# Kernel optimization log

Hardware: AMD Instinct MI355X
Metric: run time of the kernel (lower is better)

The kernel has to match this reference:

```python
import jax, jax.numpy as jnp
import numpy as np

N_NODES = 100000
N_EDGES = 1200000
D = 64          # node_feat_size
G_FEAT = 128    # graph_feat_size
N_GRAPHS = 256
N_TASKS = 1


def setup_inputs() -> dict:
    key = jax.random.key(0)
    ks = jax.random.split(key, 12)
    node_feats = jax.random.normal(ks[0], (N_NODES, D), dtype=jnp.float32)
    edge_feats = jax.random.normal(ks[1], (N_EDGES, 8), dtype=jnp.float32)
    src = jax.random.randint(ks[2], (N_EDGES,), 0, N_NODES, dtype=jnp.int64 if jax.config.read('jax_enable_x64') else jnp.int32)
    dst = jax.random.randint(ks[3], (N_EDGES,), 0, N_NODES, dtype=src.dtype)
    graph_ids = jnp.sort(jax.random.randint(ks[4], (N_NODES,), 0, N_GRAPHS, dtype=src.dtype))
    s = 1.0 / np.sqrt(D)
    W_gcn = jax.random.uniform(ks[5], (D, D), minval=-s, maxval=s, dtype=jnp.float32)
    b_gcn = jnp.zeros((D,), jnp.float32)
    W_res = jax.random.uniform(ks[6], (D, D), minval=-s, maxval=s, dtype=jnp.float32)
    b_res = jnp.zeros((D,), jnp.float32)
    W_in = jax.random.uniform(ks[7], (D, D), minval=-s, maxval=s, dtype=jnp.float32)
    b_in = jnp.zeros((D,), jnp.float32)
    W_out = jax.random.uniform(ks[8], (D, G_FEAT), minval=-s, maxval=s, dtype=jnp.float32)
    b_out = jnp.zeros((G_FEAT,), jnp.float32)
    sp = 1.0 / np.sqrt(G_FEAT)
    W_pred = jax.random.uniform(ks[9], (G_FEAT, N_TASKS), minval=-sp, maxval=sp, dtype=jnp.float32)
    b_pred = jnp.zeros((N_TASKS,), jnp.float32)
    return dict(node_feats=node_feats, edge_feats=edge_feats, src=src, dst=dst,
                graph_ids=graph_ids, W_gcn=W_gcn, b_gcn=b_gcn, W_res=W_res, b_res=b_res,
                W_in=W_in, b_in=b_in, W_out=W_out, b_out=b_out, W_pred=W_pred, b_pred=b_pred)


def reference(node_feats, edge_feats, src, dst, graph_ids,
              W_gcn, b_gcn, W_res, b_res, W_in, b_in, W_out, b_out, W_pred, b_pred):
    # --- GCNLayer (GraphConv norm='none', activation=relu, residual=True) ---
    # message passing: copy src features, sum at dst (no normalization)
    agg = jax.ops.segment_sum(node_feats[src], dst, num_segments=N_NODES)  # [N, D]
    h = jax.nn.relu(agg @ W_gcn + b_gcn)                                   # graph_conv output
    h = h + jax.nn.relu(node_feats @ W_res + b_res)                        # residual branch
    # --- MLPNodeReadout (mode='sum') ---
    h = jax.nn.relu(h @ W_in + b_in)      # [N, D]
    h = h @ W_out + b_out                 # [N, G_FEAT]
    g_feats = jax.ops.segment_sum(h, graph_ids, num_segments=N_GRAPHS)  # [G, G_FEAT]
    # --- predict ---
    out = (g_feats @ W_pred + b_pred).reshape(-1)  # [G * n_tasks]
    return out
```

## Files before the change

### kernel.cpp

```cpp
#include <hip/hip_runtime.h>

typedef __attribute__((ext_vector_type(8))) __bf16 bf16x8;
typedef __attribute__((ext_vector_type(4))) float f32x4;

union Frag { unsigned short u[8]; bf16x8 b; };

__device__ __forceinline__ unsigned short rne_bf16(float x) {
    unsigned int u = __float_as_uint(x);
    return (unsigned short)((u + 0x7fffu + ((u >> 16) & 1u)) >> 16);
}
__device__ __forceinline__ float bf16_to_f(unsigned short h) {
    return __uint_as_float(((unsigned int)h) << 16);
}

#define MFMA16 __builtin_amdgcn_mfma_f32_16x16x32_bf16
#define BSH 7
#define BNODES 128
#define BCAP 2048
#define BINCHUNK 4096
#define NWFRAG (3 * 2 * 2 * 4 * 64 * 8)

__global__ __launch_bounds__(256) void prepbin_kernel(
    const float* __restrict__ nf, const int* __restrict__ src,
    const int* __restrict__ dst,
    const float* __restrict__ Wg, const float* __restrict__ Wr,
    const float* __restrict__ Wi, const float* __restrict__ Wo,
    const float* __restrict__ bo, const float* __restrict__ Wp,
    const float* __restrict__ bp,
    unsigned short* __restrict__ nfb, unsigned short* __restrict__ wfrag,
    float* __restrict__ wfold, float* __restrict__ c0, float* __restrict__ out,
    int* __restrict__ gcursor, int* __restrict__ binned,
    int nBin, int nE, int nb, int out_size, int nNodes) {
    __shared__ int lhist[800], lbase[800], lpos[800];
    const int t = threadIdx.x;
    if ((int)blockIdx.x < nBin) {
        for (int i = t; i < nb; i += 256) { lhist[i] = 0; lpos[i] = 0; }
        __syncthreads();
        const int e0 = blockIdx.x * BINCHUNK;
        const int e1 = min(e0 + BINCHUNK, nE);
        for (int e = e0 + t; e < e1; e += 256)
            atomicAdd(&lhist[dst[e] >> BSH], 1);
        __syncthreads();
        for (int i = t; i < nb; i += 256) {
            int c = lhist[i];
            lbase[i] = c ? atomicAdd(&gcursor[i], c) : 0;
        }
        __syncthreads();
        for (int e = e0 + t; e < e1; e += 256) {
            int d = dst[e];
            int bkt = d >> BSH;
            int p = atomicAdd(&lpos[bkt], 1);
            int gp = lbase[bkt] + p;
            if (gp < BCAP) binned[bkt * BCAP + gp] = (src[e] << BSH) | (d & (BNODES - 1));
        }
        return;
    }
    const int tp = ((int)blockIdx.x - nBin) * 256 + t;
    const int nth = ((int)gridDim.x - nBin) * 256;
    const float4* nf4 = (const float4*)nf;
    ushort4* nfb4 = (ushort4*)nfb;
    const int nQ = nNodes * 16;
    for (int i = tp; i < nQ; i += nth) {
        float4 v = nf4[i];
        ushort4 o;
        o.x = rne_bf16(v.x); o.y = rne_bf16(v.y);
        o.z = rne_bf16(v.z); o.w = rne_bf16(v.w);
        nfb4[i] = o;
    }
    const float* Ws[3] = {Wg, Wr, Wi};
    for (int idx = tp; idx < NWFRAG; idx += nth) {
        int j = idx & 7, lane = (idx >> 3) & 63, nt = (idx >> 9) & 3;
        int kt = (idx >> 11) & 1, part = (idx >> 12) & 1, mat = idx >> 13;
        int k = kt * 32 + ((lane >> 4) << 3) + j;
        int n = nt * 16 + (lane & 15);
        float w = Ws[mat][k * 64 + n];
        unsigned short hi = rne_bf16(w);
        wfrag[idx] = (part == 0) ? hi : rne_bf16(w - bf16_to_f(hi));
    }
    if (tp < 64) {
        float s = 0.f;
        for (int j = 0; j < 128; ++j) s += Wo[tp * 128 + j] * Wp[j];
        wfold[tp] = s;
    }
    if (tp == 0) {
        float s = 0.f;
        for (int j = 0; j < 128; ++j) s += bo[j] * Wp[j];
        c0[0] = s;
    }
    if (tp < out_size) out[tp] = bp[0];
}

__global__ __launch_bounds__(256) void seg_kernel(
    int* __restrict__ binned, const int* __restrict__ gcursor,
    int2* __restrict__ nodeTab, int nNodes) {
    __shared__ int eL[BCAP];
    __shared__ int deg[BNODES], sc[BNODES], cur[BNODES];
    const int b = blockIdx.x, t = threadIdx.x;
    const int cnt = min(gcursor[b], BCAP);
    if (t < BNODES) deg[t] = 0;
    __syncthreads();
    for (int i = t; i < cnt; i += 256) {
        int p = binned[b * BCAP + i];
        eL[i] = p;
        atomicAdd(&deg[p & (BNODES - 1)], 1);
    }
    __syncthreads();
    if (t < BNODES) sc[t] = deg[t];
    __syncthreads();
    #pragma unroll
    for (int s = 1; s < BNODES; s <<= 1) {
        int v = 0;
        if (t < BNODES && t >= s) v = sc[t - s];
        __syncthreads();
        if (t < BNODES) sc[t] += v;
        __syncthreads();
    }
    if (t < BNODES) {
        int excl = sc[t] - deg[t];
        cur[t] = excl;
        int node = b * BNODES + t;
        if (node < nNodes) nodeTab[node] = make_int2(b * BCAP + excl, deg[t]);
    }
    __syncthreads();
    for (int i = t; i < cnt; i += 256) {
        int p = eL[i];
        int pos = atomicAdd(&cur[p & (BNODES - 1)], 1);
        binned[b * BCAP + pos] = p >> BSH;
    }
}

__global__ __launch_bounds__(256) void gather_kernel(
    const unsigned short* __restrict__ nfb, const int2* __restrict__ nodeTab,
    const int* __restrict__ srcs, unsigned short* __restrict__ aggb, int nNodes) {
    int wid = blockIdx.x * 4 + (threadIdx.x >> 6);
    if (wid >= nNodes) return;
    int lane = threadIdx.x & 63;
    int half = lane >> 5;
    int cp = lane & 31;
    int2 sd = nodeTab[wid];
    int base = sd.x, d = sd.y;
    const ushort2* nfb2 = (const ushort2*)nfb;
    float ax = 0.f, ay = 0.f;
    int k = half;
    for (; k + 8 <= d; k += 8) {
        int s0 = srcs[base + k],     s1 = srcs[base + k + 2];
        int s2 = srcs[base + k + 4], s3 = srcs[base + k + 6];
        ushort2 v0 = nfb2[(long)s0 * 32 + cp];
        ushort2 v1 = nfb2[(long)s1 * 32 + cp];
        ushort2 v2 = nfb2[(long)s2 * 32 + cp];
        ushort2 v3 = nfb2[(long)s3 * 32 + cp];
        ax += (bf16_to_f(v0.x) + bf16_to_f(v1.x)) + (bf16_to_f(v2.x) + bf16_to_f(v3.x));
        ay += (bf16_to_f(v0.y) + bf16_to_f(v1.y)) + (bf16_to_f(v2.y) + bf16_to_f(v3.y));
    }
    for (; k < d; k += 2) {
        int s = srcs[base + k];
        ushort2 v = nfb2[(long)s * 32 + cp];
        ax += bf16_to_f(v.x); ay += bf16_to_f(v.y);
    }
    ax += __shfl_xor(ax, 32, 64);
    ay += __shfl_xor(ay, 32, 64);
    if (half == 0) {
        ushort2 o; o.x = rne_bf16(ax); o.y = rne_bf16(ay);
        ((ushort2*)aggb)[(long)wid * 32 + cp] = o;
    }
}

__global__ __launch_bounds__(256) void mlp_kernel(
    const unsigned short* __restrict__ aggb, const unsigned short* __restrict__ nfb,
    const int* __restrict__ gids, const unsigned short* __restrict__ wfrag,
    const float* __restrict__ bg, const float* __restrict__ br,
    const float* __restrict__ bi, const float* __restrict__ wfold,
    const float* __restrict__ c0p, float* __restrict__ out, int nTiles) {
    __shared__ float hs_all[4][32 * 68];
    const int wave = threadIdx.x >> 6, lane = threadIdx.x & 63;
    const int wid = blockIdx.x * 4 + wave;
    if (wid >= nTiles) return;
    float* hs = hs_all[wave];
    const int base = wid * 32;
    const int mrow = lane & 15, quad = lane >> 4;

    Frag aA[2][2], aN[2][2];
    #pragma unroll
    for (int rt = 0; rt < 2; ++rt) {
        const unsigned short* rowA = aggb + (long)(base + rt * 16 + mrow) * 64;
        const unsigned short* rowN = nfb  + (long)(base + rt * 16 + mrow) * 64;
        #pragma unroll
        for (int kt = 0; kt < 2; ++kt) {
            aA[rt][kt].b = *(const bf16x8*)(rowA + kt * 32 + quad * 8);
            aN[rt][kt].b = *(const bf16x8*)(rowN + kt * 32 + quad * 8);
        }
    }

    const unsigned short* wl0 = wfrag + lane * 8;
    auto WF = [&](int mat, int part, int kt, int nt) -> bf16x8 {
        return *(const bf16x8*)(wl0 + (size_t)((((mat * 2 + part) * 2 + kt) * 4 + nt) * 64) * 8);
    };

    f32x4 accA[2][4], accR[2][4];
    #pragma unroll
    for (int rt = 0; rt < 2; ++rt)
        #pragma unroll
        for (int nt = 0; nt < 4; ++nt) {
            accA[rt][nt] = (f32x4){0.f, 0.f, 0.f, 0.f};
            accR[rt][nt] = (f32x4){0.f, 0.f, 0.f, 0.f};
        }
    #pragma unroll
    for (int nt = 0; nt < 4; ++nt)
        #pragma unroll
        for (int kt = 0; kt < 2; ++kt) {
            bf16x8 gh = WF(0, 0, kt, nt), gl = WF(0, 1, kt, nt);
            bf16x8 rh = WF(1, 0, kt, nt), rl = WF(1, 1, kt, nt);
            #pragma unroll
            for (int rt = 0; rt < 2; ++rt) {
                accA[rt][nt] = MFMA16(aA[rt][kt].b, gh, accA[rt][nt], 0, 0, 0);
                accA[rt][nt] = MFMA16(aA[rt][kt].b, gl, accA[rt][nt], 0, 0, 0);
                accR[rt][nt] = MFMA16(aN[rt][kt].b, rh, accR[rt][nt], 0, 0, 0);
                accR[rt][nt] = MFMA16(aN[rt][kt].b, rl, accR[rt][nt], 0, 0, 0);
            }
        }

    #pragma unroll
    for (int nt = 0; nt < 4; ++nt) {
        float bgv = bg[nt * 16 + mrow], brv = br[nt * 16 + mrow];
        #pragma unroll
        for (int rt = 0; rt < 2; ++rt)
            #pragma unroll
            for (int r = 0; r < 4; ++r) {
                float h = fmaxf(accA[rt][nt][r] + bgv, 0.f)
                        + fmaxf(accR[rt][nt][r] + brv, 0.f);
                hs[(rt * 16 + quad * 4 + r) * 68 + nt * 16 + mrow] = h;
            }
    }
    __builtin_amdgcn_wave_barrier();

    Frag aH[2][2];
    #pragma unroll
    for (int rt = 0; rt < 2; ++rt)
        #pragma unroll
        for (int kt = 0; kt < 2; ++kt) {
            const float* hp = hs + (rt * 16 + mrow) * 68 + kt * 32 + quad * 8;
            float4 v0 = *(const float4*)hp;
            float4 v1 = *(const float4*)(hp + 4);
            aH[rt][kt].u[0] = rne_bf16(v0.x); aH[rt][kt].u[1] = rne_bf16(v0.y);
            aH[rt][kt].u[2] = rne_bf16(v0.z); aH[rt][kt].u[3] = rne_bf16(v0.w);
            aH[rt][kt].u[4] = rne_bf16(v1.x); aH[rt][kt].u[5] = rne_bf16(v1.y);
            aH[rt][kt].u[6] = rne_bf16(v1.z); aH[rt][kt].u[7] = rne_bf16(v1.w);
        }
    f32x4 accH[2][4];
    #pragma unroll
    for (int rt = 0; rt < 2; ++rt)
        #pragma unroll
        for (int nt = 0; nt < 4; ++nt)
            accH[rt][nt] = (f32x4){0.f, 0.f, 0.f, 0.f};
    #pragma unroll
    for (int nt = 0; nt < 4; ++nt)
        #pragma unroll
        for (int kt = 0; kt < 2; ++kt) {
            bf16x8 ih = WF(2, 0, kt, nt), il = WF(2, 1, kt, nt);
            #pragma unroll
            for (int rt = 0; rt < 2; ++rt) {
                accH[rt][nt] = MFMA16(aH[rt][kt].b, ih, accH[rt][nt], 0, 0, 0);
                accH[rt][nt] = MFMA16(aH[rt][kt].b, il, accH[rt][nt], 0, 0, 0);
            }
        }

    float p[2][4];
    #pragma unroll
    for (int rt = 0; rt < 2; ++rt)
        #pragma unroll
        for (int r = 0; r < 4; ++r) p[rt][r] = 0.f;
    #pragma unroll
    for (int nt = 0; nt < 4; ++nt) {
        float biv = bi[nt * 16 + mrow], wfv = wfold[nt * 16 + mrow];
        #pragma unroll
        for (int rt = 0; rt < 2; ++rt)
            #pragma unroll
            for (int r = 0; r < 4; ++r)
                p[rt][r] += fmaxf(accH[rt][nt][r] + biv, 0.f) * wfv;
    }
    #pragma unroll
    for (int m = 1; m <= 8; m <<= 1)
        #pragma unroll
        for (int rt = 0; rt < 2; ++rt)
            #pragma unroll
            for (int r = 0; r < 4; ++r)
                p[rt][r] += __shfl_xor(p[rt][r], m, 64);
    const float c0 = c0p[0];
    #pragma unroll
    for (int rt = 0; rt < 2; ++rt)
        #pragma unroll
        for (int r = 0; r < 4; ++r) p[rt][r] += c0;

    int gself = gids[base + (lane & 31)];
    int g0 = __shfl(gself, 0, 64);
    if (__all(gself == g0)) {
        float pv = 0.f;
        if (mrow == 0) {
            #pragma unroll
            for (int rt = 0; rt < 2; ++rt)
                #pragma unroll
                for (int r = 0; r < 4; ++r) pv += p[rt][r];
        }
        pv += __shfl_xor(pv, 16, 64);
        pv += __shfl_xor(pv, 32, 64);
        if (lane == 0) atomicAdd(out + g0, pv);
    } else if (mrow == 0) {
        #pragma unroll
        for (int rt = 0; rt < 2; ++rt)
            #pragma unroll
            for (int r = 0; r < 4; ++r)
                atomicAdd(out + gids[base + rt * 16 + quad * 4 + r], p[rt][r]);
    }
}

extern "C" void kernel_launch(void* const* d_in, const int* in_sizes, int n_in,
                              void* d_out, int out_size, void* d_ws, size_t ws_size,
                              hipStream_t stream) {
    const float* node_feats = (const float*)d_in[0];
    const int* src  = (const int*)d_in[2];
    const int* dst  = (const int*)d_in[3];
    const int* gids = (const int*)d_in[4];
    const float* Wg = (const float*)d_in[5];
    const float* bg = (const float*)d_in[6];
    const float* Wr = (const float*)d_in[7];
    const float* br = (const float*)d_in[8];
    const float* Wi = (const float*)d_in[9];
    const float* bi = (const float*)d_in[10];
    const float* Wo = (const float*)d_in[11];
    const float* bo = (const float*)d_in[12];
    const float* Wp = (const float*)d_in[13];
    const float* bp = (const float*)d_in[14];
    float* out = (float*)d_out;

    const int nNodes = in_sizes[0] / 64;
    const int nE = in_sizes[2];
    const int nb = (nNodes + BNODES - 1) / BNODES;

    int* gcursor = (int*)d_ws;
    int* binned  = gcursor + 1024;
    int2* nodeTab = (int2*)(binned + (size_t)nb * BCAP);
    unsigned short* nfb  = (unsigned short*)(nodeTab + nNodes);
    unsigned short* aggb = nfb + (size_t)nNodes * 64;
    unsigned short* wfrag = aggb + (size_t)nNodes * 64;
    float* wfold = (float*)(wfrag + NWFRAG);
    float* c0 = wfold + 64;

    hipMemsetAsync(gcursor, 0, 1024 * sizeof(int), stream);

    const int nBin = (nE + BINCHUNK - 1) / BINCHUNK;
    prepbin_kernel<<<nBin + 512, 256, 0, stream>>>(
        node_feats, src, dst, Wg, Wr, Wi, Wo, bo, Wp, bp,
        nfb, wfrag, wfold, c0, out, gcursor, binned,
        nBin, nE, nb, out_size, nNodes);

    seg_kernel<<<nb, 256, 0, stream>>>(binned, gcursor, nodeTab, nNodes);
    gather_kernel<<<(nNodes + 3) / 4, 256, 0, stream>>>(nfb, nodeTab, binned, aggb, nNodes);

    const int nTiles = (nNodes + 31) / 32;
    mlp_kernel<<<(nTiles + 3) / 4, 256, 0, stream>>>(aggb, nfb, gids, wfrag,
        bg, br, bi, wfold, c0, out, nTiles);
}
```

Before: 233.4 us.

## Bin edges into 1024-node superbuckets and segment with 1024-thread blocks

Edge binning now groups destinations into about 98 buckets of 1024 nodes each instead of about 782 buckets of 128 nodes. This cuts the number of per-block global cursor atomics and shrinks the shared-memory histograms. The segment kernel now runs one 1024-thread block per superbucket, with a larger shared edge list and a 1024-wide scan. Binning blocks no longer return early, so every block in the prep kernel also takes part in the bf16 conversion and weight-fragment work. The cost is that the segment stage launches only about 98 blocks on a GPU with many CUs. Each block also does a longer scan, and the per-bucket capacity leaves little headroom over the expected edge count.

```diff
diff --git a/kernel.cpp b/kernel.cpp
--- a/kernel.cpp
+++ b/kernel.cpp
@@ -14,13 +14,13 @@
 }
 
 #define MFMA16 __builtin_amdgcn_mfma_f32_16x16x32_bf16
-#define BSH 7
-#define BNODES 128
-#define BCAP 2048
+#define SBSH 10
+#define SBN 1024
+#define SBCAP 13056
 #define BINCHUNK 4096
 #define NWFRAG (3 * 2 * 2 * 4 * 64 * 8)
 
-__global__ __launch_bounds__(256) void prepbin_kernel(
+__global__ __launch_bounds__(256) void prepbinA_kernel(
     const float* __restrict__ nf, const int* __restrict__ src,
     const int* __restrict__ dst,
     const float* __restrict__ Wg, const float* __restrict__ Wr,
@@ -30,33 +30,32 @@
     unsigned short* __restrict__ nfb, unsigned short* __restrict__ wfrag,
     float* __restrict__ wfold, float* __restrict__ c0, float* __restrict__ out,
     int* __restrict__ gcursor, int* __restrict__ binned,
-    int nBin, int nE, int nb, int out_size, int nNodes) {
-    __shared__ int lhist[800], lbase[800], lpos[800];
+    int nBin, int nE, int nbS, int out_size, int nNodes) {
+    __shared__ int lhist[128], lbase[128], lpos[128];
     const int t = threadIdx.x;
     if ((int)blockIdx.x < nBin) {
-        for (int i = t; i < nb; i += 256) { lhist[i] = 0; lpos[i] = 0; }
+        for (int i = t; i < nbS; i += 256) { lhist[i] = 0; lpos[i] = 0; }
         __syncthreads();
         const int e0 = blockIdx.x * BINCHUNK;
         const int e1 = min(e0 + BINCHUNK, nE);
         for (int e = e0 + t; e < e1; e += 256)
-            atomicAdd(&lhist[dst[e] >> BSH], 1);
-        __syncthreads();
-        for (int i = t; i < nb; i += 256) {
+            atomicAdd(&lhist[dst[e] >> SBSH], 1);
+        __syncthreads();
+        for (int i = t; i < nbS; i += 256) {
             int c = lhist[i];
             lbase[i] = c ? atomicAdd(&gcursor[i], c) : 0;
         }
         __syncthreads();
         for (int e = e0 + t; e < e1; e += 256) {
             int d = dst[e];
-            int bkt = d >> BSH;
-            int p = atomicAdd(&lpos[bkt], 1);
-            int gp = lbase[bkt] + p;
-            if (gp < BCAP) binned[bkt * BCAP + gp] = (src[e] << BSH) | (d & (BNODES - 1));
-        }
-        return;
-    }
-    const int tp = ((int)blockIdx.x - nBin) * 256 + t;
-    const int nth = ((int)gridDim.x - nBin) * 256;
+            int sb = d >> SBSH;
+            int p = atomicAdd(&lpos[sb], 1);
+            int gp = lbase[sb] + p;
+            if (gp < SBCAP) binned[sb * SBCAP + gp] = (src[e] << SBSH) | (d & (SBN - 1));
+        }
+    }
+    const int tp = (int)blockIdx.x * 256 + t;
+    const int nth = (int)gridDim.x * 256;
     const float4* nf4 = (const float4*)nf;
     ushort4* nfb4 = (ushort4*)nfb;
     const int nQ = nNodes * 16;
@@ -90,42 +89,41 @@
     if (tp < out_size) out[tp] = bp[0];
 }
 
-__global__ __launch_bounds__(256) void seg_kernel(
+__global__ __launch_bounds__(1024) void segB_kernel(
     int* __restrict__ binned, const int* __restrict__ gcursor,
     int2* __restrict__ nodeTab, int nNodes) {
-    __shared__ int eL[BCAP];
-    __shared__ int deg[BNODES], sc[BNODES], cur[BNODES];
+    __shared__ int eL[SBCAP];
+    __shared__ int deg[SBN], sc[SBN], cur[SBN];
     const int b = blockIdx.x, t = threadIdx.x;
-    const int cnt = min(gcursor[b], BCAP);
-    if (t < BNODES) deg[t] = 0;
+    const int cnt = min(gcursor[b], SBCAP);
+    deg[t] = 0;
     __syncthreads();
-    for (int i = t; i < cnt; i += 256) {
-        int p = binned[b * BCAP + i];
+    for (int i = t; i < cnt; i += 1024) {
+        int p = binned[b * SBCAP + i];
         eL[i] = p;
-        atomicAdd(&deg[p & (BNODES - 1)], 1);
+        atomicAdd(&deg[p & (SBN - 1)], 1);
     }
     __syncthreads();
-    if (t < BNODES) sc[t] = deg[t];
+    sc[t] = deg[t];
     __syncthreads();
     #pragma unroll
-    for (int s = 1; s < BNODES; s <<= 1) {
-        int v = 0;
-        if (t < BNODES && t >= s) v = sc[t - s];
-        __syncthreads();
-        if (t < BNODES) sc[t] += v;
-        __syncthreads();
-    }
-    if (t < BNODES) {
+    for (int s = 1; s < SBN; s <<= 1) {
+        int v = (t >= s) ? sc[t - s] : 0;
+        __syncthreads();
+        sc[t] += v;
+        __syncthreads();
+    }
+    {
         int excl = sc[t] - deg[t];
         cur[t] = excl;
-        int node = b * BNODES + t;
-        if (node < nNodes) nodeTab[node] = make_int2(b * BCAP + excl, deg[t]);
+        int node = b * SBN + t;
+        if (node < nNodes) nodeTab[node] = make_int2(b * SBCAP + excl, deg[t]);
     }
     __syncthreads();
-    for (int i = t; i < cnt; i += 256) {
+    for (int i = t; i < cnt; i += 1024) {
         int p = eL[i];
-        int pos = atomicAdd(&cur[p & (BNODES - 1)], 1);
-        binned[b * BCAP + pos] = p >> BSH;
+        int pos = atomicAdd(&cur[p & (SBN - 1)], 1);
+        binned[b * SBCAP + pos] = p >> SBSH;
     }
 }
 
@@ -334,26 +332,27 @@
 
     const int nNodes = in_sizes[0] / 64;
     const int nE = in_sizes[2];
-    const int nb = (nNodes + BNODES - 1) / BNODES;
+    const int nbS = (nNodes + SBN - 1) / SBN;
 
     int* gcursor = (int*)d_ws;
-    int* binned  = gcursor + 1024;
-    int2* nodeTab = (int2*)(binned + (size_t)nb * BCAP);
+    int* binned  = gcursor + 128;
+    int2* nodeTab = (int2*)(binned + (size_t)nbS * SBCAP);
     unsigned short* nfb  = (unsigned short*)(nodeTab + nNodes);
     unsigned short* aggb = nfb + (size_t)nNodes * 64;
     unsigned short* wfrag = aggb + (size_t)nNodes * 64;
     float* wfold = (float*)(wfrag + NWFRAG);
     float* c0 = wfold + 64;
 
-    hipMemsetAsync(gcursor, 0, 1024 * sizeof(int), stream);
+    hipMemsetAsync(gcursor, 0, 128 * sizeof(int), stream);
 
     const int nBin = (nE + BINCHUNK - 1) / BINCHUNK;
-    prepbin_kernel<<<nBin + 512, 256, 0, stream>>>(
+    prepbinA_kernel<<<nBin + 512, 256, 0, stream>>>(
         node_feats, src, dst, Wg, Wr, Wi, Wo, bo, Wp, bp,
         nfb, wfrag, wfold, c0, out, gcursor, binned,
-        nBin, nE, nb, out_size, nNodes);
-
-    seg_kernel<<<nb, 256, 0, stream>>>(binned, gcursor, nodeTab, nNodes);
+        nBin, nE, nbS, out_size, nNodes);
+
+    segB_kernel<<<nbS, 1024, 0, stream>>>(binned, gcursor, nodeTab, nNodes);
+
     gather_kernel<<<(nNodes + 3) / 4, 256, 0, stream>>>(nfb, nodeTab, binned, aggb, nNodes);
 
     const int nTiles = (nNodes + 31) / 32;
```

Measured after the change: 231.7 us. No clear change (-0.7%).
